# Kernel tuning notes

Hardware: AMD Instinct MI355X
Metric: run time of the kernel (lower is better)

## Reference

```python
import jax, jax.numpy as jnp
import numpy as np

NHEAD, DK, DV, DMODEL, L = 8, 64, 64, 512, 32

def setup_inputs() -> dict:
    key = jax.random.key(0)
    ks = jax.random.split(key, 9)
    B, N = 4, 2048
    s = 1.0 / np.sqrt(DMODEL)
    return {
        "q": jax.random.normal(ks[0], (B, N, DMODEL), jnp.float32),
        "k": jax.random.normal(ks[1], (B, N, DMODEL), jnp.float32),
        "v": jax.random.normal(ks[2], (B, N, DMODEL), jnp.float32),
        "Wq": jax.random.normal(ks[3], (DMODEL, NHEAD * DK), jnp.float32) * s,
        "Wk": jax.random.normal(ks[4], (DMODEL, NHEAD * DK), jnp.float32) * s,
        "Wv": jax.random.normal(ks[5], (DMODEL, NHEAD * DV), jnp.float32) * s,
        "Wfc": jax.random.normal(ks[6], (NHEAD * DV, DMODEL), jnp.float32) * s,
        "ln_g": jnp.ones((DMODEL,), jnp.float32),
        "ln_b": jnp.zeros((DMODEL,), jnp.float32),
    }

def reference(q, k, v, Wq, Wk, Wv, Wfc, ln_g, ln_b):
    B, Nq, _ = q.shape
    residual = q
    # project and split heads: [B, H, N, d]
    qh = (q @ Wq).reshape(B, Nq, NHEAD, DK).transpose(0, 2, 1, 3)
    kh = (k @ Wk).reshape(B, k.shape[1], NHEAD, DK).transpose(0, 2, 1, 3)
    vh = (v @ Wv).reshape(B, v.shape[1], NHEAD, DV).transpose(0, 2, 1, 3)
    # scaled dot-product scores and softmax over keys
    attn = jnp.einsum('bhqd,bhkd->bhqk', qh / jnp.sqrt(jnp.float32(DK)), kh)
    attn = jax.nn.softmax(attn, axis=-1)
    # AWG: keep entries >= l-th largest per row, renormalize
    threshold = jax.lax.top_k(attn, L)[0][..., -1:]  # [B,H,Nq,1]
    W = jnp.where(attn >= threshold, attn, 0.0)
    W_out = W / jnp.sum(W, axis=-1, keepdims=True)
    out = jnp.einsum('bhqk,bhkd->bhqd', W_out, vh)
    out = out.transpose(0, 2, 1, 3).reshape(B, Nq, NHEAD * DV)
    out = out @ Wfc + residual
    # LayerNorm, eps=1e-6
    mu = jnp.mean(out, axis=-1, keepdims=True)
    var = jnp.var(out, axis=-1, keepdims=True)
    return (out - mu) / jnp.sqrt(var + 1e-6) * ln_g + ln_b
```

## Files before the change

kernel.cpp:

```cpp
#include <hip/hip_runtime.h>
#include <hip/hip_fp16.h>

#define BATCH 4
#define NSEQ 2048
#define DMODEL 512
#define NHEAD 8
#define HDIM 64
#define LSEL 32
#define SROWU 2056
#define MAXL 64
#define QROWS 16
#define CSTRIDE 165

typedef __attribute__((ext_vector_type(8))) _Float16 f16x8;
typedef __attribute__((ext_vector_type(4))) float f32x4;
typedef unsigned long long ull;

__device__ inline ushort f2h(float x) { __half h = __float2half(x); return *reinterpret_cast<ushort*>(&h); }
__device__ inline float h16f(ushort u) { __half t; *reinterpret_cast<ushort*>(&t) = u; return __half2float(t); }
__device__ inline float sort2f(uint su) {
    ushort hb = (su & 0x8000u) ? (ushort)(su ^ 0x8000u) : (ushort)(su ^ 0xFFFFu);
    return h16f(hb);
}
__device__ inline uint sm2(uint w) {
    uint s = (w >> 15) & 0x00010001u;
    uint m = s * 0x7FFFu;
    return w ^ (m | 0x80008000u);
}

__global__ __launch_bounds__(256) void cvtA_kernel(
    const float* __restrict__ q, const float* __restrict__ k, const float* __restrict__ v,
    ushort* __restrict__ q16, ushort* __restrict__ k16, ushort* __restrict__ v16)
{
    const int z = blockIdx.y;
    const float* src = (z == 0) ? q : (z == 1) ? k : v;
    ushort* dst = (z == 0) ? q16 : (z == 1) ? k16 : v16;
    const size_t base = (size_t)blockIdx.x * 2048 + threadIdx.x * 4;
    float4 fa = *(const float4*)(src + base);
    float4 fb = *(const float4*)(src + base + 1024);
    ushort4 ha = {f2h(fa.x), f2h(fa.y), f2h(fa.z), f2h(fa.w)};
    ushort4 hb = {f2h(fb.x), f2h(fb.y), f2h(fb.z), f2h(fb.w)};
    *(ushort4*)(dst + base) = ha;
    *(ushort4*)(dst + base + 1024) = hb;
}

__global__ __launch_bounds__(256) void cvtW_kernel(
    const float* __restrict__ Wq, const float* __restrict__ Wk,
    const float* __restrict__ Wv, const float* __restrict__ Wfc,
    ushort* __restrict__ Wt)
{
    const int z = blockIdx.y;
    const float* W = (z == 0) ? Wq : (z == 1) ? Wk : (z == 2) ? Wv : Wfc;
    ushort* O = Wt + (size_t)z * DMODEL * DMODEL;
    const int gt = blockIdx.x * 256 + threadIdx.x;
    const int n = gt & 511;
    const int kc = (gt >> 9) * 16;
    uint pk[8];
#pragma unroll
    for (int i = 0; i < 8; ++i) {
        uint lo = f2h(W[(size_t)(kc + 2 * i) * DMODEL + n]);
        uint hi = f2h(W[(size_t)(kc + 2 * i + 1) * DMODEL + n]);
        pk[i] = lo | (hi << 16);
    }
    uint4 u0 = {pk[0], pk[1], pk[2], pk[3]};
    uint4 u1 = {pk[4], pk[5], pk[6], pk[7]};
    *(uint4*)(O + (size_t)n * DMODEL + kc) = u0;
    *(uint4*)(O + (size_t)n * DMODEL + kc + 8) = u1;
}

template<int MODE>
__global__ __launch_bounds__(256, 2) void hgemm_kernel(
    const ushort* __restrict__ A0, const ushort* __restrict__ A1, const ushort* __restrict__ A2,
    const ushort* __restrict__ Wt,
    ushort* __restrict__ O0, ushort* __restrict__ O1, ushort* __restrict__ O2,
    float* __restrict__ Ofc)
{
    __shared__ ushort Ah[64][40];
    __shared__ ushort Bh[512][40];

    const int tid = threadIdx.x;
    const int wave = tid >> 6, lane = tid & 63;
    const int lr = lane & 15, lg = lane >> 4;
    const int bm = blockIdx.x * 64;
    const int z = blockIdx.y;

    const ushort* A16 = (MODE == 0) ? (z == 0 ? A0 : z == 1 ? A1 : A2) : A0;
    const ushort* Wz = Wt + (size_t)((MODE == 0) ? z : 3) * (DMODEL * DMODEL);

    f32x4 acc[4][8];
#pragma unroll
    for (int i = 0; i < 4; ++i)
#pragma unroll
        for (int j = 0; j < 8; ++j) acc[i][j] = (f32x4){0.f, 0.f, 0.f, 0.f};

    const int sar = tid >> 2, sak = (tid & 3) * 8;

    for (int k0 = 0; k0 < DMODEL; k0 += 32) {
        __syncthreads();
        *(uint4*)&Ah[sar][sak] = *(const uint4*)(A16 + (size_t)(bm + sar) * DMODEL + k0 + sak);
#pragma unroll
        for (int i = 0; i < 8; ++i) {
            int n = sar + 64 * i;
            *(uint4*)&Bh[n][sak] = *(const uint4*)(Wz + (size_t)n * DMODEL + k0 + sak);
        }
        __syncthreads();
        f16x8 af[4];
#pragma unroll
        for (int fr = 0; fr < 4; ++fr) af[fr] = *(const f16x8*)&Ah[fr * 16 + lr][lg * 8];
#pragma unroll
        for (int fc2 = 0; fc2 < 8; ++fc2) {
            f16x8 bf = *(const f16x8*)&Bh[wave * 128 + fc2 * 16 + lr][lg * 8];
#pragma unroll
            for (int fr = 0; fr < 4; ++fr)
                acc[fr][fc2] = __builtin_amdgcn_mfma_f32_16x16x32_f16(af[fr], bf, acc[fr][fc2], 0, 0, 0);
        }
    }

    if (MODE == 1) {
#pragma unroll
        for (int fr = 0; fr < 4; ++fr)
#pragma unroll
            for (int fc2 = 0; fc2 < 8; ++fc2)
#pragma unroll
                for (int r = 0; r < 4; ++r)
                    Ofc[(size_t)(bm + fr * 16 + lg * 4 + r) * DMODEL + wave * 128 + fc2 * 16 + lr] = acc[fr][fc2][r];
        return;
    }

    const float osc = (z == 0) ? 0.125f : 1.0f;
    ushort* O = (z == 0) ? O0 : (z == 1) ? O1 : O2;
    const int b = bm >> 11;
    const int nseq0 = bm & (NSEQ - 1);
    ushort* smw = (ushort*)&Bh[0][0] + wave * (64 * 72);
#pragma unroll
    for (int hp = 0; hp < 2; ++hp) {
        __syncthreads();
#pragma unroll
        for (int f4 = 0; f4 < 4; ++f4) {
            int fc2 = hp * 4 + f4;
            int nl = f4 * 16 + lr;
#pragma unroll
            for (int fr = 0; fr < 4; ++fr)
#pragma unroll
                for (int r = 0; r < 4; ++r)
                    smw[(fr * 16 + lg * 4 + r) * 72 + nl] = f2h(acc[fr][fc2][r] * osc);
        }
        __syncthreads();
        const int h = wave * 2 + hp;
        ushort* obase = O + ((size_t)(b * NHEAD + h) * NSEQ + nseq0) * HDIM;
#pragma unroll
        for (int i = 0; i < 8; ++i) {
            int m = i * 8 + (lane >> 3);
            int dc = (lane & 7) * 8;
            *(uint4*)(obase + (size_t)m * HDIM + dc) = *(const uint4*)(smw + m * 72 + dc);
        }
    }
}

__device__ inline int wave_sum6(int c) {
    int tot = (int)__popcll(__ballot(c & 1));
    tot += (int)__popcll(__ballot(c & 2)) << 1;
    tot += (int)__popcll(__ballot(c & 4)) << 2;
    tot += (int)__popcll(__ballot(c & 8)) << 3;
    tot += (int)__popcll(__ballot(c & 16)) << 4;
    tot += (int)__popcll(__ballot(c & 32)) << 5;
    return tot;
}

__device__ uint full_thr(const ushort* Sr, int lane, uint lo0) {
    uint flo = lo0, fhi = 0xFFFFu;
#pragma unroll 1
    for (int it2 = 0; it2 < 16; ++it2) {
        uint mid = (flo + fhi + 1) >> 1, M = mid << 16;
        int cl = 0;
#pragma unroll
        for (int it = 0; it < 4; ++it) {
            uint4 r4 = *(const uint4*)(Sr + it * 512 + lane * 8);
            cl += ((r4.x << 16) >= M) + ((r4.x & 0xFFFF0000u) >= M);
            cl += ((r4.y << 16) >= M) + ((r4.y & 0xFFFF0000u) >= M);
            cl += ((r4.z << 16) >= M) + ((r4.z & 0xFFFF0000u) >= M);
            cl += ((r4.w << 16) >= M) + ((r4.w & 0xFFFF0000u) >= M);
        }
        bool ge = wave_sum6(cl) >= LSEL;
        flo = ge ? mid : flo;
        fhi = ge ? fhi : mid - 1;
    }
    return flo;
}

__device__ int recount(const ushort* Sr, int lane, uint th) {
    int cs = 0;
#pragma unroll
    for (int it = 0; it < 4; ++it) {
        uint4 r4 = *(const uint4*)(Sr + it * 512 + lane * 8);
        cs += ((r4.x << 16) >= th) + ((r4.x & 0xFFFF0000u) >= th);
        cs += ((r4.y << 16) >= th) + ((r4.y & 0xFFFF0000u) >= th);
        cs += ((r4.z << 16) >= th) + ((r4.z & 0xFFFF0000u) >= th);
        cs += ((r4.w << 16) >= th) + ((r4.w & 0xFFFF0000u) >= th);
    }
    return cs;
}

__device__ float extract_big(const ushort* Sr, int lane, uint th, float Mv,
                             int pre, uint* selrow)
{
    const float L2E = 1.4426950408889634f;
    float wp = 0.f;
    int pos = pre;
#pragma unroll
    for (int it = 0; it < 4; ++it) {
        uint4 r4 = *(const uint4*)(Sr + it * 512 + lane * 8);
        uint ib = (uint)(it * 512 + lane * 8);
        uint wds[4] = {r4.x, r4.y, r4.z, r4.w};
#pragma unroll
        for (int c = 0; c < 4; ++c) {
            uint vL = wds[c] << 16, vH = wds[c] & 0xFFFF0000u;
            if (vL >= th) {
                ushort w16 = f2h(exp2f((sort2f(vL >> 16) - Mv) * L2E));
                if (pos < MAXL) { selrow[pos] = ((uint)w16 << 16) | (ib + c * 2); wp += h16f(w16); }
                ++pos;
            }
            if (vH >= th) {
                ushort w16 = f2h(exp2f((sort2f(vH >> 16) - Mv) * L2E));
                if (pos < MAXL) { selrow[pos] = ((uint)w16 << 16) | (ib + c * 2 + 1); wp += h16f(w16); }
                ++pos;
            }
        }
    }
#pragma unroll
    for (int off = 32; off >= 1; off >>= 1) wp += __shfl_xor(wp, off);
    return wp;
}

#define INS5(T0, T1, T2, T3, T4, P) { \
    uint m1_ = min(P, T0); T0 = max(P, T0); \
    uint m2_ = min(m1_, T1); T1 = max(m1_, T1); \
    uint m3_ = min(m2_, T2); T2 = max(m2_, T2); \
    uint m4_ = min(m3_, T3); T3 = max(m3_, T3); \
    T4 = max(m4_, T4); }

__global__ __launch_bounds__(512, 4) void attn_kernel(
    const ushort* __restrict__ qh, const ushort* __restrict__ kh,
    const ushort* __restrict__ vh, ushort* __restrict__ ao)
{
    __shared__ __align__(16) ushort Sbuf[QROWS * SROWU];
    __shared__ uint cand[QROWS * CSTRIDE];
    __shared__ __align__(16) uint sel[QROWS][MAXL];

    const int tid = threadIdx.x;
    const int wave = tid >> 6;
    const int lane = tid & 63;
    const int bh = blockIdx.y;
    const int q0 = blockIdx.x * QROWS;
    const int lr = lane & 15;
    const int lg = lane >> 4;
    const float L2E = 1.4426950408889634f;

    const ushort* Qb = qh + ((size_t)bh * NSEQ + q0) * HDIM;
    const ushort* Kb = kh + (size_t)bh * NSEQ * HDIM;

    f16x8 qf0 = *(const f16x8*)(Qb + lr * HDIM + lg * 8);
    f16x8 qf1 = *(const f16x8*)(Qb + lr * HDIM + 32 + lg * 8);

    uint u00 = 0, u01 = 0, u02 = 0, u03 = 0, u04 = 0;
    uint u10 = 0, u11 = 0, u12 = 0, u13 = 0, u14 = 0;
    uint u20 = 0, u21 = 0, u22 = 0, u23 = 0, u24 = 0;
    uint u30 = 0, u31 = 0, u32 = 0, u33 = 0, u34 = 0;

    const int kwbase = wave * 256;
    const ushort* Kt0 = Kb + (size_t)kwbase * HDIM;
    f16x8 a0 = *(const f16x8*)(Kt0 + lr * HDIM + lg * 8);
    f16x8 a1 = *(const f16x8*)(Kt0 + lr * HDIM + 32 + lg * 8);

#pragma unroll
    for (int t = 0; t < 16; ++t) {
        f16x8 n0 = a0, n1 = a1;
        if (t < 15) {
            const ushort* Kn = Kb + (size_t)(kwbase + (t + 1) * 16) * HDIM;
            n0 = *(const f16x8*)(Kn + lr * HDIM + lg * 8);
            n1 = *(const f16x8*)(Kn + lr * HDIM + 32 + lg * 8);
        }
        f32x4 acc = {0.f, 0.f, 0.f, 0.f};
        acc = __builtin_amdgcn_mfma_f32_16x16x32_f16(a0, qf0, acc, 0, 0, 0);
        acc = __builtin_amdgcn_mfma_f32_16x16x32_f16(a1, qf1, acc, 0, 0, 0);
        const uint col = (uint)(kwbase + t * 16 + lg * 4);
        uint w0 = (uint)f2h(acc[0]) | ((uint)f2h(acc[1]) << 16);
        uint w1 = (uint)f2h(acc[2]) | ((uint)f2h(acc[3]) << 16);
        w0 = sm2(w0); w1 = sm2(w1);
        uint2 pk = {w0, w1};
        *(uint2*)&Sbuf[lr * SROWU + col] = pk;
        uint p;
        p = (w0 << 16) | col;               INS5(u00, u01, u02, u03, u04, p);
        p = (w0 & 0xFFFF0000u) | (col + 1); INS5(u10, u11, u12, u13, u14, p);
        p = (w1 << 16) | (col + 2);         INS5(u20, u21, u22, u23, u24, p);
        p = (w1 & 0xFFFF0000u) | (col + 3); INS5(u30, u31, u32, u33, u34, p);
        a0 = n0; a1 = n1;
    }

    INS5(u00, u01, u02, u03, u04, u10); INS5(u00, u01, u02, u03, u04, u11);
    INS5(u00, u01, u02, u03, u04, u12); INS5(u00, u01, u02, u03, u04, u13);
    INS5(u00, u01, u02, u03, u04, u14);
    INS5(u00, u01, u02, u03, u04, u20); INS5(u00, u01, u02, u03, u04, u21);
    INS5(u00, u01, u02, u03, u04, u22); INS5(u00, u01, u02, u03, u04, u23);
    INS5(u00, u01, u02, u03, u04, u24);
    INS5(u00, u01, u02, u03, u04, u30); INS5(u00, u01, u02, u03, u04, u31);
    INS5(u00, u01, u02, u03, u04, u32); INS5(u00, u01, u02, u03, u04, u33);
    INS5(u00, u01, u02, u03, u04, u34);

    {
        const int sidx = wave * 4 + lg;
        const int cb = lr * CSTRIDE + sidx;
        cand[cb +   0] = u00;
        cand[cb +  33] = u01;
        cand[cb +  66] = u02;
        cand[cb +  99] = u03;
        cand[cb + 132] = u04;
    }
    __syncthreads();

    const int halfid = lane >> 5;
    const int s = lane & 31;
    const int qrA = wave * 2, qrB = qrA + 1;
    const int qrMy = qrA + halfid;
    const int b = bh >> 3, hh = bh & 7;

    uint c0, c1, c2, c3, c4;
    {
        const int cb = qrMy * CSTRIDE + s;
        c0 = cand[cb]; c1 = cand[cb + 33]; c2 = cand[cb + 66];
        c3 = cand[cb + 99]; c4 = cand[cb + 132];
    }

    uint mx = c0;
#pragma unroll
    for (int off = 1; off <= 16; off <<= 1) mx = max(mx, (uint)__shfl_xor((int)mx, off));
    const float Mv = sort2f(mx >> 16);

    uint lo = 0, hi = 0xFFFFu;
#pragma unroll
    for (int it = 0; it < 16; ++it) {
        uint mid = (lo + hi + 1) >> 1, M = mid << 16;
        int cnt = (c0 >= M) + (c1 >= M) + (c2 >= M) + (c3 >= M) + (c4 >= M);
        ull m0 = __ballot(cnt & 1), m1 = __ballot(cnt & 2), m2 = __ballot(cnt & 4);
        int tA = (int)__popcll(m0 & 0xFFFFFFFFull) + 2 * (int)__popcll(m1 & 0xFFFFFFFFull)
               + 4 * (int)__popcll(m2 & 0xFFFFFFFFull);
        int tB = (int)__popcll(m0 >> 32) + 2 * (int)__popcll(m1 >> 32) + 4 * (int)__popcll(m2 >> 32);
        bool ge = (halfid ? tB : tA) >= LSEL;
        lo = ge ? mid : lo;
        hi = ge ? hi : mid - 1;
    }
    uint th = lo << 16;

    const float MvA = __shfl(Mv, 0), MvB = __shfl(Mv, 32);
    const uint loA = (uint)__shfl((int)lo, 0), loB = (uint)__shfl((int)lo, 32);

    ull mm = __ballot(c4 >= th);
    const bool missA = (mm & 0xFFFFFFFFull) != 0ull;
    const bool missB = (mm >> 32) != 0ull;
    const bool myMiss = halfid ? missB : missA;

    float wsMy = 1.f;
    int nkMy = 0;

    if (!myMiss) {
        int cs = (c0 >= th) + (c1 >= th) + (c2 >= th) + (c3 >= th);
        ull HB = halfid ? 0xFFFFFFFF00000000ull : 0x00000000FFFFFFFFull;
        ull below = ((1ull << lane) - 1ull) & HB;
        int pre = 0, tot = 0;
#pragma unroll
        for (int bb = 0; bb < 3; ++bb) {
            ull m = __ballot((cs >> bb) & 1);
            pre += (int)__popcll(m & below) << bb;
            tot += (int)__popcll(m & HB) << bb;
        }
        float wp = 0.f;
        uint cc0 = c0, cc1 = c1, cc2 = c2, cc3 = c3;
#pragma unroll
        for (int i = 0; i < 4; ++i) {
            uint ci = (i == 0) ? cc0 : (i == 1) ? cc1 : (i == 2) ? cc2 : cc3;
            if (ci >= th) {
                ushort w16 = f2h(exp2f((sort2f(ci >> 16) - Mv) * L2E));
                int pos = pre + i;
                if (pos < MAXL) { sel[qrMy][pos] = ((uint)w16 << 16) | (ci & 0xFFFFu); wp += h16f(w16); }
            }
        }
#pragma unroll
        for (int off = 1; off <= 16; off <<= 1) wp += __shfl_xor(wp, off);
        wsMy = wp;
        nkMy = (tot < MAXL) ? tot : MAXL;
    }

    if (missA) {
        const ushort* Sr = &Sbuf[qrA * SROWU];
        uint ft = full_thr(Sr, lane, loA);
        uint thv = ft << 16;
        int cs = recount(Sr, lane, thv);
        ull below64 = (1ull << lane) - 1ull;
        int preS = 0, totS = 0;
#pragma unroll
        for (int bb = 0; bb < 6; ++bb) {
            ull m = __ballot((cs >> bb) & 1);
            preS += (int)__popcll(m & below64) << bb;
            totS += (int)__popcll(m) << bb;
        }
        float wa = extract_big(Sr, lane, thv, MvA, preS, &sel[qrA][0]);
        if (halfid == 0) { wsMy = wa; nkMy = (totS < MAXL) ? totS : MAXL; }
    }
    if (missB) {
        const ushort* Sr = &Sbuf[qrB * SROWU];
        uint ft = full_thr(Sr, lane, loB);
        uint thv = ft << 16;
        int cs = recount(Sr, lane, thv);
        ull below64 = (1ull << lane) - 1ull;
        int preS = 0, totS = 0;
#pragma unroll
        for (int bb = 0; bb < 6; ++bb) {
            ull m = __ballot((cs >> bb) & 1);
            preS += (int)__popcll(m & below64) << bb;
            totS += (int)__popcll(m) << bb;
        }
        float wb = extract_big(Sr, lane, thv, MvB, preS, &sel[qrB][0]);
        if (halfid == 1) { wsMy = wb; nkMy = (totS < MAXL) ? totS : MAXL; }
    }

    asm volatile("s_waitcnt lgkmcnt(0)" ::: "memory");

    const __half2* V2 = reinterpret_cast<const __half2*>(vh + (size_t)bh * NSEQ * HDIM);
    const int dp = lane & 31;
    const uint* selp = &sel[qrMy][0];

    float ox = 0.f, oy = 0.f;
    int j = 0;
    for (; j + 8 <= nkMy; j += 8) {
        uint e[8];
        *(uint4*)&e[0] = *(const uint4*)(selp + j);
        *(uint4*)&e[4] = *(const uint4*)(selp + j + 4);
        float2 vv[8];
        float ww[8];
#pragma unroll
        for (int i2 = 0; i2 < 8; ++i2) {
            int idx = (int)(e[i2] & 0xFFFFu);
            ww[i2] = h16f((ushort)(e[i2] >> 16));
            vv[i2] = __half22float2(V2[(size_t)idx * 32 + dp]);
        }
#pragma unroll
        for (int i2 = 0; i2 < 8; ++i2) { ox += ww[i2] * vv[i2].x; oy += ww[i2] * vv[i2].y; }
    }
    for (; j < nkMy; ++j) {
        uint e = selp[j];
        int idx = (int)(e & 0xFFFFu);
        float w = h16f((ushort)(e >> 16));
        float2 v0 = __half22float2(V2[(size_t)idx * 32 + dp]);
        ox += w * v0.x; oy += w * v0.y;
    }

    const float inv = 1.f / wsMy;
    uint opk = (uint)f2h(ox * inv) | ((uint)f2h(oy * inv) << 16);
    *(uint*)(ao + ((size_t)(b * NSEQ) + q0 + qrMy) * DMODEL + hh * HDIM + dp * 2) = opk;
}

__global__ __launch_bounds__(256) void ln_kernel(
    const float* __restrict__ fcr, const float* __restrict__ resid,
    const float* __restrict__ g, const float* __restrict__ bta, float* __restrict__ out)
{
    const int row = blockIdx.x * 4 + (threadIdx.x >> 6);
    const int lane = threadIdx.x & 63;
    const size_t base = (size_t)row * DMODEL + lane * 8;
    float4 xa = *(const float4*)(fcr + base);
    float4 xb = *(const float4*)(fcr + base + 4);
    float4 ra = *(const float4*)(resid + base);
    float4 rb = *(const float4*)(resid + base + 4);
    xa.x += ra.x; xa.y += ra.y; xa.z += ra.z; xa.w += ra.w;
    xb.x += rb.x; xb.y += rb.y; xb.z += rb.z; xb.w += rb.w;
    float sum = xa.x + xa.y + xa.z + xa.w + xb.x + xb.y + xb.z + xb.w;
    float sq = xa.x * xa.x + xa.y * xa.y + xa.z * xa.z + xa.w * xa.w
             + xb.x * xb.x + xb.y * xb.y + xb.z * xb.z + xb.w * xb.w;
#pragma unroll
    for (int off = 32; off >= 1; off >>= 1) {
        sum += __shfl_xor(sum, off);
        sq += __shfl_xor(sq, off);
    }
    float mean = sum * (1.f / 512.f);
    float var = sq * (1.f / 512.f) - mean * mean;
    float rstd = rsqrtf(var + 1e-6f);
    float4 ga = *(const float4*)(g + lane * 8);
    float4 gb = *(const float4*)(g + lane * 8 + 4);
    float4 ba = *(const float4*)(bta + lane * 8);
    float4 bb = *(const float4*)(bta + lane * 8 + 4);
    float4 oa, ob;
    oa.x = (xa.x - mean) * rstd * ga.x + ba.x;
    oa.y = (xa.y - mean) * rstd * ga.y + ba.y;
    oa.z = (xa.z - mean) * rstd * ga.z + ba.z;
    oa.w = (xa.w - mean) * rstd * ga.w + ba.w;
    ob.x = (xb.x - mean) * rstd * gb.x + bb.x;
    ob.y = (xb.y - mean) * rstd * gb.y + bb.y;
    ob.z = (xb.z - mean) * rstd * gb.z + bb.z;
    ob.w = (xb.w - mean) * rstd * gb.w + bb.w;
    *(float4*)(out + base) = oa;
    *(float4*)(out + base + 4) = ob;
}

extern "C" void kernel_launch(void* const* d_in, const int* in_sizes, int n_in,
                              void* d_out, int out_size, void* d_ws, size_t ws_size,
                              hipStream_t stream)
{
    (void)in_sizes; (void)n_in; (void)out_size; (void)ws_size;

    const float* q   = (const float*)d_in[0];
    const float* k   = (const float*)d_in[1];
    const float* v   = (const float*)d_in[2];
    const float* Wq  = (const float*)d_in[3];
    const float* Wk  = (const float*)d_in[4];
    const float* Wv  = (const float*)d_in[5];
    const float* Wfc = (const float*)d_in[6];
    const float* g   = (const float*)d_in[7];
    const float* b   = (const float*)d_in[8];
    float* out = (float*)d_out;

    const size_t SZ = (size_t)BATCH * NSEQ * DMODEL;
    const size_t WSZ = (size_t)DMODEL * DMODEL;
    ushort* w16 = (ushort*)d_ws;
    ushort* q16 = w16;
    ushort* k16 = w16 + SZ;
    ushort* v16 = w16 + 2 * SZ;
    ushort* Wt  = w16 + 3 * SZ;
    ushort* qh  = Wt + 4 * WSZ;
    ushort* kh  = qh + SZ;
    ushort* vh  = kh + SZ;
    ushort* ao  = vh + SZ;
    float* fc_raw = (float*)d_ws;

    cvtA_kernel<<<dim3(2048, 3), 256, 0, stream>>>(q, k, v, q16, k16, v16);
    cvtW_kernel<<<dim3(64, 4), 256, 0, stream>>>(Wq, Wk, Wv, Wfc, Wt);
    hgemm_kernel<0><<<dim3(128, 3), 256, 0, stream>>>(q16, k16, v16, Wt, qh, kh, vh, nullptr);
    attn_kernel<<<dim3(NSEQ / QROWS, BATCH * NHEAD), 512, 0, stream>>>(qh, kh, vh, ao);
    hgemm_kernel<1><<<dim3(128, 1), 256, 0, stream>>>(ao, nullptr, nullptr, Wt, nullptr, nullptr, nullptr, fc_raw);
    ln_kernel<<<(BATCH * NSEQ) / 4, 256, 0, stream>>>(fc_raw, q, g, b, out);
}
```

Baseline: 324.7 us.

## Drop full score buffer in LDS; recompute scores for rare overflow rows

Removes the 16x2056 fp16 score buffer (~66KB LDS) from the attention kernel. When a row's top-5 candidate lists overflow, that row's scores are recomputed with MFMA into a single-row buffer. The per-lane candidate lists are also merged from four 5-deep lists into two, which writes twice as many candidates to shared memory and gives more work to the binary-search count. Less LDS allows raising launch bounds to 8 blocks per CU. The trade-off is redundant QK recomputation plus extra block-wide barriers whenever any row misses.

```diff
diff --git a/kernel.cpp b/kernel.cpp
--- a/kernel.cpp
+++ b/kernel.cpp
@@ -7,10 +7,9 @@
 #define NHEAD 8
 #define HDIM 64
 #define LSEL 32
-#define SROWU 2056
 #define MAXL 64
 #define QROWS 16
-#define CSTRIDE 165
+#define CSTRIDE 331
 
 typedef __attribute__((ext_vector_type(8))) _Float16 f16x8;
 typedef __attribute__((ext_vector_type(4))) float f32x4;
@@ -239,13 +238,16 @@
     uint m4_ = min(m3_, T3); T3 = max(m3_, T3); \
     T4 = max(m4_, T4); }
 
-__global__ __launch_bounds__(512, 4) void attn_kernel(
+__global__ __launch_bounds__(512, 8) void attn_kernel(
     const ushort* __restrict__ qh, const ushort* __restrict__ kh,
     const ushort* __restrict__ vh, ushort* __restrict__ ao)
 {
-    __shared__ __align__(16) ushort Sbuf[QROWS * SROWU];
     __shared__ uint cand[QROWS * CSTRIDE];
     __shared__ __align__(16) uint sel[QROWS][MAXL];
+    __shared__ __align__(16) ushort Sb1[2056];
+    __shared__ float wsums[QROWS];
+    __shared__ int   nks[QROWS];
+    __shared__ int   missflag[QROWS];
 
     const int tid = threadIdx.x;
     const int wave = tid >> 6;
@@ -262,10 +264,8 @@
     f16x8 qf0 = *(const f16x8*)(Qb + lr * HDIM + lg * 8);
     f16x8 qf1 = *(const f16x8*)(Qb + lr * HDIM + 32 + lg * 8);
 
-    uint u00 = 0, u01 = 0, u02 = 0, u03 = 0, u04 = 0;
-    uint u10 = 0, u11 = 0, u12 = 0, u13 = 0, u14 = 0;
-    uint u20 = 0, u21 = 0, u22 = 0, u23 = 0, u24 = 0;
-    uint u30 = 0, u31 = 0, u32 = 0, u33 = 0, u34 = 0;
+    uint sA0 = 0, sA1 = 0, sA2 = 0, sA3 = 0, sA4 = 0;
+    uint sB0 = 0, sB1 = 0, sB2 = 0, sB3 = 0, sB4 = 0;
 
     const int kwbase = wave * 256;
     const ushort* Kt0 = Kb + (size_t)kwbase * HDIM;
@@ -287,51 +287,41 @@
         uint w0 = (uint)f2h(acc[0]) | ((uint)f2h(acc[1]) << 16);
         uint w1 = (uint)f2h(acc[2]) | ((uint)f2h(acc[3]) << 16);
         w0 = sm2(w0); w1 = sm2(w1);
-        uint2 pk = {w0, w1};
-        *(uint2*)&Sbuf[lr * SROWU + col] = pk;
         uint p;
-        p = (w0 << 16) | col;               INS5(u00, u01, u02, u03, u04, p);
-        p = (w0 & 0xFFFF0000u) | (col + 1); INS5(u10, u11, u12, u13, u14, p);
-        p = (w1 << 16) | (col + 2);         INS5(u20, u21, u22, u23, u24, p);
-        p = (w1 & 0xFFFF0000u) | (col + 3); INS5(u30, u31, u32, u33, u34, p);
+        p = (w0 << 16) | col;               INS5(sA0, sA1, sA2, sA3, sA4, p);
+        p = (w0 & 0xFFFF0000u) | (col + 1); INS5(sA0, sA1, sA2, sA3, sA4, p);
+        p = (w1 << 16) | (col + 2);         INS5(sB0, sB1, sB2, sB3, sB4, p);
+        p = (w1 & 0xFFFF0000u) | (col + 3); INS5(sB0, sB1, sB2, sB3, sB4, p);
         a0 = n0; a1 = n1;
     }
 
-    INS5(u00, u01, u02, u03, u04, u10); INS5(u00, u01, u02, u03, u04, u11);
-    INS5(u00, u01, u02, u03, u04, u12); INS5(u00, u01, u02, u03, u04, u13);
-    INS5(u00, u01, u02, u03, u04, u14);
-    INS5(u00, u01, u02, u03, u04, u20); INS5(u00, u01, u02, u03, u04, u21);
-    INS5(u00, u01, u02, u03, u04, u22); INS5(u00, u01, u02, u03, u04, u23);
-    INS5(u00, u01, u02, u03, u04, u24);
-    INS5(u00, u01, u02, u03, u04, u30); INS5(u00, u01, u02, u03, u04, u31);
-    INS5(u00, u01, u02, u03, u04, u32); INS5(u00, u01, u02, u03, u04, u33);
-    INS5(u00, u01, u02, u03, u04, u34);
-
     {
-        const int sidx = wave * 4 + lg;
-        const int cb = lr * CSTRIDE + sidx;
-        cand[cb +   0] = u00;
-        cand[cb +  33] = u01;
-        cand[cb +  66] = u02;
-        cand[cb +  99] = u03;
-        cand[cb + 132] = u04;
+        const int sid = wave * 8 + lg * 2;
+        const int cb = lr * CSTRIDE + sid;
+        cand[cb +   0] = sA0; cand[cb +  66] = sA1; cand[cb + 132] = sA2;
+        cand[cb + 198] = sA3; cand[cb + 264] = sA4;
+        cand[cb +   1] = sB0; cand[cb +  67] = sB1; cand[cb + 133] = sB2;
+        cand[cb + 199] = sB3; cand[cb + 265] = sB4;
     }
     __syncthreads();
 
     const int halfid = lane >> 5;
     const int s = lane & 31;
-    const int qrA = wave * 2, qrB = qrA + 1;
-    const int qrMy = qrA + halfid;
+    const int qr = wave * 2 + halfid;
     const int b = bh >> 3, hh = bh & 7;
-
-    uint c0, c1, c2, c3, c4;
+    const ull LOMASK = 0xFFFFFFFFull;
+    const ull HB = halfid ? ~LOMASK : LOMASK;
+
+    uint c0, c1, c2, c3, c4, c5, c6, c7, c8, c9;
     {
-        const int cb = qrMy * CSTRIDE + s;
-        c0 = cand[cb]; c1 = cand[cb + 33]; c2 = cand[cb + 66];
-        c3 = cand[cb + 99]; c4 = cand[cb + 132];
-    }
-
-    uint mx = c0;
+        const int cb = qr * CSTRIDE + s;
+        c0 = cand[cb];       c1 = cand[cb +  66]; c2 = cand[cb + 132];
+        c3 = cand[cb + 198]; c4 = cand[cb + 264];
+        c5 = cand[cb + 32];       c6 = cand[cb +  66 + 32]; c7 = cand[cb + 132 + 32];
+        c8 = cand[cb + 198 + 32]; c9 = cand[cb + 264 + 32];
+    }
+
+    uint mx = max(c0, c5);
 #pragma unroll
     for (int off = 1; off <= 16; off <<= 1) mx = max(mx, (uint)__shfl_xor((int)mx, off));
     const float Mv = sort2f(mx >> 16);
@@ -340,94 +330,98 @@
 #pragma unroll
     for (int it = 0; it < 16; ++it) {
         uint mid = (lo + hi + 1) >> 1, M = mid << 16;
-        int cnt = (c0 >= M) + (c1 >= M) + (c2 >= M) + (c3 >= M) + (c4 >= M);
-        ull m0 = __ballot(cnt & 1), m1 = __ballot(cnt & 2), m2 = __ballot(cnt & 4);
-        int tA = (int)__popcll(m0 & 0xFFFFFFFFull) + 2 * (int)__popcll(m1 & 0xFFFFFFFFull)
-               + 4 * (int)__popcll(m2 & 0xFFFFFFFFull);
-        int tB = (int)__popcll(m0 >> 32) + 2 * (int)__popcll(m1 >> 32) + 4 * (int)__popcll(m2 >> 32);
-        bool ge = (halfid ? tB : tA) >= LSEL;
+        int cnt = (c0 >= M) + (c1 >= M) + (c2 >= M) + (c3 >= M) + (c4 >= M)
+                + (c5 >= M) + (c6 >= M) + (c7 >= M) + (c8 >= M) + (c9 >= M);
+        ull m0 = __ballot(cnt & 1), m1 = __ballot(cnt & 2);
+        ull m2 = __ballot(cnt & 4), m3 = __ballot(cnt & 8);
+        int tH = (int)__popcll(m0 & HB) + 2 * (int)__popcll(m1 & HB)
+               + 4 * (int)__popcll(m2 & HB) + 8 * (int)__popcll(m3 & HB);
+        bool ge = tH >= LSEL;
         lo = ge ? mid : lo;
         hi = ge ? hi : mid - 1;
     }
-    uint th = lo << 16;
-
-    const float MvA = __shfl(Mv, 0), MvB = __shfl(Mv, 32);
-    const uint loA = (uint)__shfl((int)lo, 0), loB = (uint)__shfl((int)lo, 32);
-
-    ull mm = __ballot(c4 >= th);
-    const bool missA = (mm & 0xFFFFFFFFull) != 0ull;
-    const bool missB = (mm >> 32) != 0ull;
-    const bool myMiss = halfid ? missB : missA;
-
-    float wsMy = 1.f;
-    int nkMy = 0;
-
-    if (!myMiss) {
-        int cs = (c0 >= th) + (c1 >= th) + (c2 >= th) + (c3 >= th);
-        ull HB = halfid ? 0xFFFFFFFF00000000ull : 0x00000000FFFFFFFFull;
+    const uint th = lo << 16;
+
+    ull mm = __ballot((c4 >= th) || (c9 >= th));
+    const bool missMy = (mm & HB) != 0ull;
+
+    if (!missMy) {
+        int csel = (c0 >= th) + (c1 >= th) + (c2 >= th) + (c3 >= th)
+                 + (c5 >= th) + (c6 >= th) + (c7 >= th) + (c8 >= th);
         ull below = ((1ull << lane) - 1ull) & HB;
         int pre = 0, tot = 0;
 #pragma unroll
-        for (int bb = 0; bb < 3; ++bb) {
-            ull m = __ballot((cs >> bb) & 1);
+        for (int bb = 0; bb < 4; ++bb) {
+            ull m = __ballot((csel >> bb) & 1);
             pre += (int)__popcll(m & below) << bb;
             tot += (int)__popcll(m & HB) << bb;
         }
+        uint regs[8] = {c0, c1, c2, c3, c5, c6, c7, c8};
         float wp = 0.f;
-        uint cc0 = c0, cc1 = c1, cc2 = c2, cc3 = c3;
-#pragma unroll
-        for (int i = 0; i < 4; ++i) {
-            uint ci = (i == 0) ? cc0 : (i == 1) ? cc1 : (i == 2) ? cc2 : cc3;
-            if (ci >= th) {
-                ushort w16 = f2h(exp2f((sort2f(ci >> 16) - Mv) * L2E));
-                int pos = pre + i;
-                if (pos < MAXL) { sel[qrMy][pos] = ((uint)w16 << 16) | (ci & 0xFFFFu); wp += h16f(w16); }
+        int k2 = 0;
+#pragma unroll
+        for (int i = 0; i < 8; ++i) {
+            uint ui = regs[i];
+            if (ui >= th) {
+                ushort w16 = f2h(exp2f((sort2f(ui >> 16) - Mv) * L2E));
+                int pos = pre + k2;
+                if (pos < MAXL) { sel[qr][pos] = ((uint)w16 << 16) | (ui & 0xFFFFu); wp += h16f(w16); }
+                ++k2;
             }
         }
 #pragma unroll
         for (int off = 1; off <= 16; off <<= 1) wp += __shfl_xor(wp, off);
-        wsMy = wp;
-        nkMy = (tot < MAXL) ? tot : MAXL;
-    }
-
-    if (missA) {
-        const ushort* Sr = &Sbuf[qrA * SROWU];
-        uint ft = full_thr(Sr, lane, loA);
-        uint thv = ft << 16;
-        int cs = recount(Sr, lane, thv);
-        ull below64 = (1ull << lane) - 1ull;
-        int preS = 0, totS = 0;
-#pragma unroll
-        for (int bb = 0; bb < 6; ++bb) {
-            ull m = __ballot((cs >> bb) & 1);
-            preS += (int)__popcll(m & below64) << bb;
-            totS += (int)__popcll(m) << bb;
-        }
-        float wa = extract_big(Sr, lane, thv, MvA, preS, &sel[qrA][0]);
-        if (halfid == 0) { wsMy = wa; nkMy = (totS < MAXL) ? totS : MAXL; }
-    }
-    if (missB) {
-        const ushort* Sr = &Sbuf[qrB * SROWU];
-        uint ft = full_thr(Sr, lane, loB);
-        uint thv = ft << 16;
-        int cs = recount(Sr, lane, thv);
-        ull below64 = (1ull << lane) - 1ull;
-        int preS = 0, totS = 0;
-#pragma unroll
-        for (int bb = 0; bb < 6; ++bb) {
-            ull m = __ballot((cs >> bb) & 1);
-            preS += (int)__popcll(m & below64) << bb;
-            totS += (int)__popcll(m) << bb;
-        }
-        float wb = extract_big(Sr, lane, thv, MvB, preS, &sel[qrB][0]);
-        if (halfid == 1) { wsMy = wb; nkMy = (totS < MAXL) ? totS : MAXL; }
-    }
-
-    asm volatile("s_waitcnt lgkmcnt(0)" ::: "memory");
+        if (s == 0) { wsums[qr] = wp; nks[qr] = (tot < MAXL) ? tot : MAXL; }
+    }
+    if (s == 0) missflag[qr] = missMy ? 1 : 0;
+    __syncthreads();
+
+    for (int r = 0; r < QROWS; ++r) {
+        if (missflag[r]) {
+            __syncthreads();
+#pragma unroll 4
+            for (int t = 0; t < 16; ++t) {
+                const ushort* Kt = Kb + (size_t)(kwbase + t * 16) * HDIM;
+                f16x8 ra0 = *(const f16x8*)(Kt + lr * HDIM + lg * 8);
+                f16x8 ra1 = *(const f16x8*)(Kt + lr * HDIM + 32 + lg * 8);
+                f32x4 ac2 = {0.f, 0.f, 0.f, 0.f};
+                ac2 = __builtin_amdgcn_mfma_f32_16x16x32_f16(ra0, qf0, ac2, 0, 0, 0);
+                ac2 = __builtin_amdgcn_mfma_f32_16x16x32_f16(ra1, qf1, ac2, 0, 0, 0);
+                if (lr == r) {
+                    uint w0 = (uint)f2h(ac2[0]) | ((uint)f2h(ac2[1]) << 16);
+                    uint w1 = (uint)f2h(ac2[2]) | ((uint)f2h(ac2[3]) << 16);
+                    uint2 pk = {sm2(w0), sm2(w1)};
+                    *(uint2*)&Sb1[kwbase + t * 16 + lg * 4] = pk;
+                }
+            }
+            __syncthreads();
+            if (wave == (r >> 1)) {
+                const int h = r & 1;
+                const float Mvr = __shfl(Mv, h * 32);
+                const uint lor = (uint)__shfl((int)lo, h * 32);
+                uint ft = full_thr(Sb1, lane, lor);
+                uint thv = ft << 16;
+                int cs = recount(Sb1, lane, thv);
+                ull below64 = (1ull << lane) - 1ull;
+                int preS = 0, totS = 0;
+#pragma unroll
+                for (int bb = 0; bb < 6; ++bb) {
+                    ull m = __ballot((cs >> bb) & 1);
+                    preS += (int)__popcll(m & below64) << bb;
+                    totS += (int)__popcll(m) << bb;
+                }
+                float wr = extract_big(Sb1, lane, thv, Mvr, preS, &sel[r][0]);
+                if (lane == 0) { wsums[r] = wr; nks[r] = (totS < MAXL) ? totS : MAXL; }
+            }
+        }
+    }
+    __syncthreads();
 
     const __half2* V2 = reinterpret_cast<const __half2*>(vh + (size_t)bh * NSEQ * HDIM);
     const int dp = lane & 31;
-    const uint* selp = &sel[qrMy][0];
+    const int nkMy = nks[qr];
+    const float wsMy = wsums[qr];
+    const uint* selp = &sel[qr][0];
 
     float ox = 0.f, oy = 0.f;
     int j = 0;
@@ -456,7 +450,7 @@
 
     const float inv = 1.f / wsMy;
     uint opk = (uint)f2h(ox * inv) | ((uint)f2h(oy * inv) << 16);
-    *(uint*)(ao + ((size_t)(b * NSEQ) + q0 + qrMy) * DMODEL + hh * HDIM + dp * 2) = opk;
+    *(uint*)(ao + ((size_t)(b * NSEQ) + q0 + qr) * DMODEL + hh * HDIM + dp * 2) = opk;
 }
 
 __global__ __launch_bounds__(256) void ln_kernel(
```

Measured after the change: 325.7 us. About the same (+0.3%).
